# Kernel optimization log

Measured on AMD Instinct MI355X. Metric: run time of the kernel, lower is better.

## Reference

```python
import jax, jax.numpy as jnp
import numpy as np

# ---- constants from init_kwargs (mode='local', channel='G') ----
MEAN = 127.5
STD = 50.0
BINS = np.array([-2.4, -1.6, -0.8, 0.0, 0.8, 1.6, 2.4])
NB = len(BINS) + 1            # 8 quantization levels
DIST = [1, 2, 3]
THETA = [0.0, np.pi / 4, np.pi / 2, 3 * np.pi / 4]
MASK = 17
STRIDE = 4
BIN_EDGES = 0.5 + BINS / 6.0
# skimage greycomatrix offsets: (round(sin(t)*d), round(cos(t)*d)), ordered d-major
OFFSETS = [(int(np.round(np.sin(t) * d)), int(np.round(np.cos(t) * d)))
           for d in DIST for t in THETA]


def setup_inputs() -> dict:
    key = jax.random.key(0)
    x = jax.random.uniform(key, (8, 3, 256, 256), dtype=jnp.float32) * 255.0
    return {"x": x}


def _features(x):
    img = x[:, 1, :, :]                       # channel 'G'
    img = jnp.where(img < 10.0, 0.0, img)     # imgs[imgs < 10] = 0
    B, H, W = img.shape
    N = (H - MASK) // STRIDE + 1              # 60 windows per axis

    # sliding windows -> (B, N, N, MASK, MASK)
    r = (jnp.arange(N) * STRIDE)[:, None] + jnp.arange(MASK)[None, :]
    win = img[:, r[:, None, :, None], r[None, :, None, :]]
    Nw = B * N * N
    flat = win.reshape(Nw, MASK * MASK)

    # ---- stat over nonzero pixels (numpy population std) ----
    mask = flat != 0.0
    n_safe = jnp.maximum(mask.sum(-1), 1).astype(flat.dtype)
    mean = jnp.where(mask, flat, 0.0).sum(-1) / n_safe
    std = jnp.sqrt((jnp.where(mask, flat - mean[:, None], 0.0) ** 2).sum(-1) / n_safe)
    mx = jnp.where(mask, flat, -jnp.inf).max(-1)
    mn = jnp.where(mask, flat, jnp.inf).min(-1)
    stat = jnp.stack([mean, std, (mx - mean) / (std + 1e-9), (mean - mn) / (std + 1e-9)], -1)

    # ---- quantize ----
    q = jnp.digitize(((flat - MEAN) / STD + 3.0) / 6.0, jnp.asarray(BIN_EDGES, flat.dtype))

    # ---- histogram (density over ALL pixels, drop first & last bin) ----
    onehot = (q[..., None] == jnp.arange(NB)).astype(flat.dtype)
    hist_feat = onehot.sum(1)[:, 1:NB - 1] / flat.shape[1]   # (Nw, len(BINS)-1)

    # ---- GLCM per (dist, theta) offset, symmetric + normed ----
    qm = q.reshape(Nw, MASK, MASK)
    rows = jnp.arange(Nw)[:, None]
    glcms = []
    for dr, dc in OFFSETS:
        if dc >= 0:
            i = qm[:, :MASK - dr, :MASK - dc]
            j = qm[:, dr:, dc:]
        else:
            i = qm[:, :MASK - dr, -dc:]
            j = qm[:, dr:, :MASK + dc]
        pair = (i * NB + j).reshape(Nw, -1)
        cnt = jnp.zeros((Nw, NB * NB), flat.dtype).at[rows, pair].add(1.0)
        P = cnt.reshape(Nw, NB, NB)
        P = P + P.transpose(0, 2, 1)                               # symmetric
        P = P / jnp.maximum(P.sum((1, 2), keepdims=True), 1e-12)   # normed
        glcms.append(P)
    G = jnp.stack(glcms, 1)          # (Nw, 12, NB, NB)
    g = G[:, :, 1:, 1:]              # crop level 0 (zeros)
    L = NB - 1

    # greycoprops renormalizes the (cropped) GLCM internally
    Pn = g / jnp.maximum(g.sum((2, 3), keepdims=True), 1e-12)
    I = jnp.arange(L, dtype=flat.dtype)
    diff2 = (I[:, None] - I[None, :]) ** 2
    contrast = (Pn * diff2).sum((2, 3))
    homog = (Pn / (1.0 + diff2)).sum((2, 3))
    energy = jnp.sqrt((Pn ** 2).sum((2, 3)))
    Pi = Pn.sum(3)
    Pj = Pn.sum(2)
    mui = (Pi * I).sum(-1)
    muj = (Pj * I).sum(-1)
    sdi = jnp.sqrt((Pi * (I - mui[..., None]) ** 2).sum(-1))
    sdj = jnp.sqrt((Pj * (I - muj[..., None]) ** 2).sum(-1))
    cov = (Pn * (I[:, None] - mui[..., None, None]) * (I[None, :] - muj[..., None, None])).sum((2, 3))
    corr = jnp.where(sdi * sdj < 1e-15, 1.0, cov / jnp.maximum(sdi * sdj, 1e-15))
    entropy = -(g * jnp.log2(g + 1e-8)).sum((2, 3))   # on cropped, non-renormed g

    glcm_feat = jnp.concatenate([contrast, homog, energy, corr, entropy], -1)  # (Nw, 60)
    feats = jnp.concatenate([stat, hist_feat, glcm_feat], -1)                  # (Nw, 70)

    # windows with max == 0 yield all-zero feature vectors
    feats = jnp.where((flat.max(-1) == 0.0)[:, None], 0.0, feats)

    Fdim = feats.shape[-1]
    feats = feats.reshape(B, N, N, Fdim)
    total = feats.sum((1, 2))
    nz = (feats != 0).sum((1, 2)).astype(flat.dtype)
    return total / (nz + 1e-9)            # (B, 70)


def reference(x):
    return _features(x)
```

## Files before the change

### kernel.cpp

```cpp
#include <hip/hip_runtime.h>
#include <cmath>

#define NPIX   289
#define NU     10
#define NF     70
#define NWX    60
#define IMG_W  256
#define IMG_HW 65536
#define NWIN   28800
#define ACC    560
#define WPB    4
#define NBLK   (NWIN / WPB)

__device__ __constant__ int c_s2u[12] = {0,1,2,3,4,1,5,3,6,7,8,9};

constexpr int DRu[NU] = {0, 1, 1, 1, 0, 2, 0, 2, 3, 2};
constexpr int DCu[NU] = {1, 1, 0,-1, 2, 0, 3, 2, 0,-2};
constexpr int JOFF[NU] = {1, 18, 17, 16, 2, 34, 3, 36, 51, 32};
constexpr float INV2N[NU] = {1.f/544.f, 1.f/512.f, 1.f/544.f, 1.f/512.f, 1.f/510.f,
                             1.f/510.f, 1.f/476.f, 1.f/450.f, 1.f/476.f, 1.f/450.f};

struct VTab { unsigned w[NU][10]; };
constexpr VTab make_vtab() {
    VTab t{};
    for (int o = 0; o < NU; ++o)
        for (int idx = 0; idx < NPIX; ++idx) {
            int r = idx / 17, c = idx % 17, cc = c + DCu[o];
            if (r + DRu[o] <= 16 && cc >= 0 && cc <= 16)
                t.w[o][idx >> 5] |= 1u << (idx & 31);
        }
    return t;
}
constexpr VTab c_vt = make_vtab();

__device__ __forceinline__ float wsum(float v){ for(int o=32;o;o>>=1) v += __shfl_xor(v,o,64); return v; }
__device__ __forceinline__ float wmax(float v){ for(int o=32;o;o>>=1) v = fmaxf(v,__shfl_xor(v,o,64)); return v; }
__device__ __forceinline__ float wmin(float v){ for(int o=32;o;o>>=1) v = fminf(v,__shfl_xor(v,o,64)); return v; }
__device__ __forceinline__ unsigned long long wsumull(unsigned long long v){
    for (int o=32;o;o>>=1) v += __shfl_xor(v,o,64); return v;
}

__global__ __launch_bounds__(256) void feat_kernel(const float* __restrict__ x,
                                                   float* __restrict__ ptot,
                                                   float* __restrict__ pnz,
                                                   int setmask) {
    __shared__ float s_g[WPB][NU * 49];
    __shared__ float s_uf[WPB][5][NU];
    __shared__ float s_s10[WPB][10];

    const int lane = threadIdx.x & 63;
    const int wid  = threadIdx.x >> 6;
    const int widx = blockIdx.x * WPB + wid;
    const int b    = widx / 3600;
    const int rem  = widx - b * 3600;
    const int wy   = rem / NWX;
    const int wx   = rem - wy * NWX;
    const float* img = x + (size_t)(b * 3 + 1) * IMG_HW + (wy * 4) * IMG_W + wx * 4;

    float* gl  = s_g[wid];
    float (*uf)[NU] = s_uf[wid];
    float* s10 = s_s10[wid];

    float v[5]; int q[5];
    float lsum = 0.f, lmax = -1e30f, lmin = 1e30f;
    unsigned long long hpack = 0ull;
#pragma unroll
    for (int k = 0; k < 5; ++k) {
        const int t = lane + k * 64;
        float val = 0.f;
        int qq = 0;
        if (t < NPIX) {
            int r = t / 17;
            int c = t - r * 17;
            float p = img[r * IMG_W + c];
            val = (p < 10.f) ? 0.f : p;
            if (val != 0.f) {
                qq = 1 + (val >= 47.5f) + (val >= 87.5f) + (val >= 127.5f)
                       + (val >= 167.5f) + (val >= 207.5f) + (val >= 247.5f);
                lsum += val;
                lmax = fmaxf(lmax, val);
                lmin = fminf(lmin, val);
                if (qq <= 6) hpack += 1ull << (9 * (qq - 1));
                hpack += 1ull << 54;
            }
        }
        v[k] = val; q[k] = qq;
    }

    const unsigned long long hp = wsumull(hpack);
    const int n = (int)(hp >> 54) & 511;
    if (n == 0) return;

    const float sum = wsum(lsum);
    const float mx  = wmax(lmax);
    const float mn  = wmin(lmin);
    const float mean = sum / (float)n;

    float lss = 0.f;
#pragma unroll
    for (int k = 0; k < 5; ++k)
        if (v[k] != 0.f) { float d = v[k] - mean; lss += d * d; }
    const float stdv = sqrtf(wsum(lss) / (float)n);

    if (lane == 0) {
        s10[0] = mean;
        s10[1] = stdv;
        s10[2] = (mx - mean) / (stdv + 1e-9f);
        s10[3] = (mean - mn) / (stdv + 1e-9f);
#pragma unroll
        for (int i = 0; i < 6; ++i)
            s10[4 + i] = (float)((hp >> (9 * i)) & 511) * (1.f / 289.f);
    }

    const int l49 = (lane < 49) ? lane : 48;
    const int ba  = l49 / 7 + 1;
    const int bb  = l49 - (ba - 1) * 7 + 1;
    unsigned ma32[10], mb32[12];
#pragma unroll
    for (int k = 0; k < 5; ++k) {
        unsigned long long p0 = __ballot(q[k] & 1);
        unsigned long long p1 = __ballot(q[k] & 2);
        unsigned long long p2 = __ballot(q[k] & 4);
        unsigned long long mA = ((ba & 1) ? p0 : ~p0) & ((ba & 2) ? p1 : ~p1) & ((ba & 4) ? p2 : ~p2);
        unsigned long long mB = ((bb & 1) ? p0 : ~p0) & ((bb & 2) ? p1 : ~p1) & ((bb & 4) ? p2 : ~p2);
        ma32[2*k]   = (unsigned)mA;  ma32[2*k+1] = (unsigned)(mA >> 32);
        mb32[2*k]   = (unsigned)mB;  mb32[2*k+1] = (unsigned)(mB >> 32);
    }
    mb32[10] = 0u; mb32[11] = 0u;

    int cnta[NU];
#pragma unroll
    for (int o = 0; o < NU; ++o) {
        const int wq = JOFF[o] >> 5;
        const int r  = JOFF[o] & 31;
        int acc = 0;
#pragma unroll
        for (int w = 0; w < 10; ++w) {
            unsigned mav = ma32[w] & c_vt.w[o][w];
            unsigned sh  = (r == 0) ? mb32[w + wq]
                 : (unsigned)(((((unsigned long long)mb32[w + wq + 1]) << 32) | mb32[w + wq]) >> r);
            acc += __popc(mav & sh);
        }
        cnta[o] = acc;
    }

    const int partner = (bb - 1) * 7 + (ba - 1);
#pragma unroll
    for (int o = 0; o < NU; ++o) {
        int pc = __shfl(cnta[o], partner, 64);
        float g = (float)(cnta[o] + pc) * INV2N[o];
        if (lane < 49) gl[o * 49 + l49] = g;
    }

    const int fo  = lane & 15;
    const int sub = lane >> 4;
    float gsum=0.f, entU=0.f, conU=0.f, homU=0.f, g2=0.f, siU=0.f, siiU=0.f, sijU=0.f;
    if (fo < NU) {
        for (int idx = sub; idx < 49; idx += 4) {
            float g = gl[fo * 49 + idx];
            int fi = idx / 7;
            int fj = idx - fi * 7;
            float d  = (float)(fi - fj);
            float d2 = d * d;
            float ffi = (float)fi, ffj = (float)fj;
            gsum += g;
            entU += g * __log2f(g + 1e-8f);
            conU += g * d2;
            homU += g * __builtin_amdgcn_rcpf(1.f + d2);
            g2   += g * g;
            siU  += g * ffi;
            siiU += g * ffi * ffi;
            sijU += g * ffi * ffj;
        }
    }
#pragma unroll
    for (int s = 16; s <= 32; s <<= 1) {
        gsum += __shfl_xor(gsum, s, 64);  entU += __shfl_xor(entU, s, 64);
        conU += __shfl_xor(conU, s, 64);  homU += __shfl_xor(homU, s, 64);
        g2   += __shfl_xor(g2,   s, 64);  siU  += __shfl_xor(siU,  s, 64);
        siiU += __shfl_xor(siiU, s, 64);  sijU += __shfl_xor(sijU, s, 64);
    }
    if (fo < NU && sub == 0) {
        const float invg = 1.f / fmaxf(gsum, 1e-12f);
        const float si  = siU  * invg;
        const float sii = siiU * invg;
        const float sij = sijU * invg;
        const float var = fmaxf(sii - si * si, 0.f);
        const float cov = sij - si * si;
        uf[0][fo] = conU * invg;
        uf[1][fo] = homU * invg;
        uf[2][fo] = sqrtf(g2) * invg;
        uf[3][fo] = (var < 1e-15f) ? 1.f : cov / fmaxf(var, 1e-15f);
        uf[4][fo] = -entU;
    }

    const int setbase = (widx & setmask) * ACC;
    const int obase   = b * NF;
    for (int t = lane; t < NF; t += 64) {
        float f;
        if (t < 10) {
            f = s10[t];
        } else {
            int u    = t - 10;
            int grp  = u / 12;
            int slot = u - grp * 12;
            f = uf[grp][c_s2u[slot]];
        }
        atomicAdd(&ptot[setbase + obase + t], f);
        if (f != 0.f) atomicAdd(&pnz[setbase + obase + t], 1.f);
    }
}

__global__ void reduce_kernel(const float* __restrict__ ptot,
                              const float* __restrict__ pnz,
                              float* __restrict__ out, int nset) {
    int t = blockIdx.x * blockDim.x + threadIdx.x;
    if (t >= ACC) return;
    float s = 0.f, nz = 0.f;
    for (int k = 0; k < nset; ++k) {
        s  += ptot[(size_t)k * ACC + t];
        nz += pnz[(size_t)k * ACC + t];
    }
    out[t] = s / (nz + 1e-9f);
}

extern "C" void kernel_launch(void* const* d_in, const int* in_sizes, int n_in,
                              void* d_out, int out_size, void* d_ws, size_t ws_size,
                              hipStream_t stream) {
    (void)in_sizes; (void)n_in; (void)out_size;
    const float* x = (const float*)d_in[0];
    float* out = (float*)d_out;

    const size_t per_set = (size_t)2 * ACC * sizeof(float);
    int maxs = (ws_size >= per_set) ? (int)(ws_size / per_set) : 1;
    int nset = 1;
    while ((nset * 2) <= maxs && nset < 64) nset <<= 1;

    float* ptot = (float*)d_ws;
    float* pnz  = ptot + (size_t)nset * ACC;

    hipMemsetAsync(d_ws, 0, (size_t)nset * per_set, stream);
    feat_kernel<<<dim3(NBLK), dim3(256), 0, stream>>>(x, ptot, pnz, nset - 1);
    reduce_kernel<<<dim3((ACC + 255) / 256), dim3(256), 0, stream>>>(ptot, pnz, out, nset);
}
```

Before: 132.9 us.

## Derive histogram counts from ballots and compute single-pass variance

Drops the 64-bit packed-histogram shuffle reduction and instead gets the non-zero count and the per-bin counts by popcounting the bit-plane ballots, which are now computed once and reused for the GLCM masks. The variance becomes a single-pass sum of squares around a fixed shift of 127.5, removing the second data pass. Quantization uses a floor-based formula instead of seven compares, and the pixel index and division-by-7 use cheaper integer arithmetic. The single-pass variance may lose some precision compared with the two-pass form.

New measurement: 125.1 us. 5.9% less time.

```diff
diff --git a/kernel.cpp b/kernel.cpp
--- a/kernel.cpp
+++ b/kernel.cpp
@@ -36,9 +36,6 @@
 __device__ __forceinline__ float wsum(float v){ for(int o=32;o;o>>=1) v += __shfl_xor(v,o,64); return v; }
 __device__ __forceinline__ float wmax(float v){ for(int o=32;o;o>>=1) v = fmaxf(v,__shfl_xor(v,o,64)); return v; }
 __device__ __forceinline__ float wmin(float v){ for(int o=32;o;o>>=1) v = fminf(v,__shfl_xor(v,o,64)); return v; }
-__device__ __forceinline__ unsigned long long wsumull(unsigned long long v){
-    for (int o=32;o;o>>=1) v += __shfl_xor(v,o,64); return v;
-}
 
 __global__ __launch_bounds__(256) void feat_kernel(const float* __restrict__ x,
                                                    float* __restrict__ ptot,
@@ -61,66 +58,74 @@
     float (*uf)[NU] = s_uf[wid];
     float* s10 = s_s10[wid];
 
-    float v[5]; int q[5];
-    float lsum = 0.f, lmax = -1e30f, lmin = 1e30f;
-    unsigned long long hpack = 0ull;
+    const int l49 = (lane < 49) ? lane : 48;
+    const int ba  = l49 / 7 + 1;
+    const int bb  = l49 - (ba - 1) * 7 + 1;
+
+    float lsum = 0.f, lss = 0.f, lmax = -1e30f, lmin = 1e30f;
+    unsigned long long p0s[5], p1s[5], p2s[5];
 #pragma unroll
     for (int k = 0; k < 5; ++k) {
         const int t = lane + k * 64;
         float val = 0.f;
-        int qq = 0;
         if (t < NPIX) {
-            int r = t / 17;
-            int c = t - r * 17;
-            float p = img[r * IMG_W + c];
+            const int r = t / 17;
+            float p = img[r * (IMG_W - 17) + t];
             val = (p < 10.f) ? 0.f : p;
-            if (val != 0.f) {
-                qq = 1 + (val >= 47.5f) + (val >= 87.5f) + (val >= 127.5f)
-                       + (val >= 167.5f) + (val >= 207.5f) + (val >= 247.5f);
-                lsum += val;
-                lmax = fmaxf(lmax, val);
-                lmin = fminf(lmin, val);
-                if (qq <= 6) hpack += 1ull << (9 * (qq - 1));
-                hpack += 1ull << 54;
-            }
-        }
-        v[k] = val; q[k] = qq;
-    }
-
-    const unsigned long long hp = wsumull(hpack);
-    const int n = (int)(hp >> 54) & 511;
+        }
+        float qf = fminf(fmaxf(floorf(fmaf(val, 0.025f, -1.1875f)) + 1.f, 0.f), 6.f);
+        int qq = (val != 0.f) ? ((int)qf + 1) : 0;
+        lsum += val;
+        float d = (val != 0.f) ? (val - 127.5f) : 0.f;
+        lss = fmaf(d, d, lss);
+        lmax = fmaxf(lmax, val);
+        lmin = fminf(lmin, (val != 0.f) ? val : 1e30f);
+        p0s[k] = __ballot(qq & 1);
+        p1s[k] = __ballot(qq & 2);
+        p2s[k] = __ballot(qq & 4);
+    }
+
+    int n = 0, c1 = 0, c2 = 0, c3 = 0, c4 = 0, c5 = 0, c6 = 0;
+#pragma unroll
+    for (int k = 0; k < 5; ++k) {
+        unsigned long long p0 = p0s[k], p1 = p1s[k], p2 = p2s[k];
+        n  += __popcll(p0 | p1 | p2);
+        c1 += __popcll(p0 & ~p1 & ~p2);
+        c2 += __popcll(~p0 & p1 & ~p2);
+        c3 += __popcll(p0 & p1 & ~p2);
+        c4 += __popcll(~p0 & ~p1 & p2);
+        c5 += __popcll(p0 & ~p1 & p2);
+        c6 += __popcll(~p0 & p1 & p2);
+    }
     if (n == 0) return;
 
-    const float sum = wsum(lsum);
-    const float mx  = wmax(lmax);
-    const float mn  = wmin(lmin);
-    const float mean = sum / (float)n;
-
-    float lss = 0.f;
-#pragma unroll
-    for (int k = 0; k < 5; ++k)
-        if (v[k] != 0.f) { float d = v[k] - mean; lss += d * d; }
-    const float stdv = sqrtf(wsum(lss) / (float)n);
+    const float fn   = (float)n;
+    const float sum  = wsum(lsum);
+    const float ss   = wsum(lss);
+    const float mx   = wmax(lmax);
+    const float mn   = wmin(lmin);
+    const float mean = sum / fn;
+    const float mc   = mean - 127.5f;
+    const float var  = fmaxf(ss / fn - mc * mc, 0.f);
+    const float stdv = sqrtf(var);
 
     if (lane == 0) {
         s10[0] = mean;
         s10[1] = stdv;
         s10[2] = (mx - mean) / (stdv + 1e-9f);
         s10[3] = (mean - mn) / (stdv + 1e-9f);
-#pragma unroll
-        for (int i = 0; i < 6; ++i)
-            s10[4 + i] = (float)((hp >> (9 * i)) & 511) * (1.f / 289.f);
-    }
-
-    const int l49 = (lane < 49) ? lane : 48;
-    const int ba  = l49 / 7 + 1;
-    const int bb  = l49 - (ba - 1) * 7 + 1;
+        s10[4] = (float)c1 * (1.f / 289.f);
+        s10[5] = (float)c2 * (1.f / 289.f);
+        s10[6] = (float)c3 * (1.f / 289.f);
+        s10[7] = (float)c4 * (1.f / 289.f);
+        s10[8] = (float)c5 * (1.f / 289.f);
+        s10[9] = (float)c6 * (1.f / 289.f);
+    }
+
     unsigned ma32[10], mb32[12];
 #pragma unroll
     for (int k = 0; k < 5; ++k) {
-        unsigned long long p0 = __ballot(q[k] & 1);
-        unsigned long long p1 = __ballot(q[k] & 2);
-        unsigned long long p2 = __ballot(q[k] & 4);
+        unsigned long long p0 = p0s[k], p1 = p1s[k], p2 = p2s[k];
         unsigned long long mA = ((ba & 1) ? p0 : ~p0) & ((ba & 2) ? p1 : ~p1) & ((ba & 4) ? p2 : ~p2);
         unsigned long long mB = ((bb & 1) ? p0 : ~p0) & ((bb & 2) ? p1 : ~p1) & ((bb & 4) ? p2 : ~p2);
         ma32[2*k]   = (unsigned)mA;  ma32[2*k+1] = (unsigned)(mA >> 32);
@@ -158,7 +163,7 @@
     if (fo < NU) {
         for (int idx = sub; idx < 49; idx += 4) {
             float g = gl[fo * 49 + idx];
-            int fi = idx / 7;
+            int fi = (idx * 37) >> 8;
             int fj = idx - fi * 7;
             float d  = (float)(fi - fj);
             float d2 = d * d;
@@ -185,12 +190,12 @@
         const float si  = siU  * invg;
         const float sii = siiU * invg;
         const float sij = sijU * invg;
-        const float var = fmaxf(sii - si * si, 0.f);
-        const float cov = sij - si * si;
+        const float varg = fmaxf(sii - si * si, 0.f);
+        const float cov  = sij - si * si;
         uf[0][fo] = conU * invg;
         uf[1][fo] = homU * invg;
         uf[2][fo] = sqrtf(g2) * invg;
-        uf[3][fo] = (var < 1e-15f) ? 1.f : cov / fmaxf(var, 1e-15f);
+        uf[3][fo] = (varg < 1e-15f) ? 1.f : cov / fmaxf(varg, 1e-15f);
         uf[4][fo] = -entU;
     }
 
```
